# Performance work log

Hardware: AMD Instinct MI355X
Metric: run time of the kernel (lower is better)

## Reference

```python
import jax, jax.numpy as jnp
import numpy as np

N = 100000       # nodes
F_IN = 512       # input features
H = 16           # hidden dim of conv1
C = 5            # num classes
E = 6400000      # edges (avg degree 64)


def setup_inputs() -> dict:
    key = jax.random.key(0)
    ks = jax.random.split(key, 8)
    x = jax.random.normal(ks[0], (N, F_IN), dtype=jnp.float32)
    edge_index = jax.random.randint(ks[1], (2, E), 0, N, dtype=jnp.int64)
    W1 = jax.random.normal(ks[2], (F_IN, H), dtype=jnp.float32) * (1.0 / np.sqrt(F_IN))
    b1 = jnp.zeros((H,), jnp.float32)
    W2 = jax.random.normal(ks[3], (H, C), dtype=jnp.float32) * (1.0 / np.sqrt(H))
    b2 = jnp.zeros((C,), jnp.float32)
    W3 = jax.random.normal(ks[4], (C, 32), dtype=jnp.float32) * (1.0 / np.sqrt(C))
    b3 = jnp.zeros((32,), jnp.float32)
    W4 = jax.random.normal(ks[5], (32, C), dtype=jnp.float32) * (1.0 / np.sqrt(32))
    b4 = jnp.zeros((C,), jnp.float32)
    return {"x": x, "edge_index": edge_index, "W1": W1, "b1": b1,
            "W2": W2, "b2": b2, "W3": W3, "b3": b3, "W4": W4, "b4": b4}


def _gcn_norm(edge_index):
    # add self-loops, unit edge weights (data has no edge_attr)
    loop = jnp.arange(N, dtype=edge_index.dtype)
    src = jnp.concatenate([edge_index[0], loop])
    dst = jnp.concatenate([edge_index[1], loop])
    deg = jax.ops.segment_sum(jnp.ones_like(dst, dtype=jnp.float32), dst,
                              num_segments=N)
    dinv = jnp.where(deg > 0, jax.lax.rsqrt(jnp.maximum(deg, 1.0)), 0.0)
    norm = dinv[src] * dinv[dst]  # [E+N]
    return src, dst, norm


def _gcn_conv(x, src, dst, norm, W, b):
    h = x @ W                               # transform first (small out dim)
    msg = h[src] * norm[:, None]            # gather + edge-normalize
    out = jax.ops.segment_sum(msg, dst, num_segments=N)  # scatter-add
    return out + b


def reference(x, edge_index, W1, b1, W2, b2, W3, b3, W4, b4):
    src, dst, norm = _gcn_norm(edge_index)
    h = _gcn_conv(x, src, dst, norm, W1, b1)
    h = jax.nn.relu(h)
    # F.dropout(training=self.training): identity in eval mode
    h = _gcn_conv(h, src, dst, norm, W2, b2)
    h = jax.nn.relu(h @ W3 + b3)
    h = h @ W4 + b4
    return jax.nn.log_softmax(h, axis=1)
```

## Files before the change

kernel.cpp:

```cpp
#include <hip/hip_runtime.h>
#include <hip/hip_bf16.h>


#define F_IN 512
#define HDIM 16
#define CDIM 5
#define NB   1024
#define SEG  8192
#define GWP_STRIDE 16
#define EPT  10
#define SCHUNK (1024*EPT)
#define CAP  8192

typedef __attribute__((ext_vector_type(8))) short short8;
typedef __attribute__((ext_vector_type(4))) float floatx4;

__device__ inline float bf2f(unsigned short u){
  unsigned int i = ((unsigned int)u) << 16; float f; __builtin_memcpy(&f, &i, 4); return f;
}
__device__ inline unsigned short f2bf(float x){
  unsigned int i; __builtin_memcpy(&i, &x, 4);
  unsigned int r = i + 0x7FFFu + ((i >> 16) & 1u);
  return (unsigned short)(r >> 16);
}
__device__ inline float ulo(unsigned int u){
  unsigned int v = u << 16; float f; __builtin_memcpy(&f, &v, 4); return f;
}
__device__ inline float uhi(unsigned int u){
  unsigned int v = u & 0xFFFF0000u; float f; __builtin_memcpy(&f, &v, 4); return f;
}
__device__ inline short8 pack8(float4 u0, float4 u1){
  unsigned short o[8] = {f2bf(u0.x), f2bf(u0.y), f2bf(u0.z), f2bf(u0.w),
                         f2bf(u1.x), f2bf(u1.y), f2bf(u1.z), f2bf(u1.w)};
  short8 r; __builtin_memcpy(&r, o, 16); return r;
}

__global__ __launch_bounds__(1024) void k_detect(const int* __restrict__ ei, int* __restrict__ flag,
                                                 int* __restrict__ gwp, const float* __restrict__ W1,
                                                 unsigned short* __restrict__ pw, int E){
  int t = threadIdx.x;
  if (t == 0) *flag = 0;
  gwp[t * GWP_STRIDE] = t * SEG;
  {
    int col = t & 15, kg = (t >> 4) & 3, tt = t >> 6;
    unsigned short o[8];
    #pragma unroll
    for (int e = 0; e < 8; ++e)
      o[e] = f2bf(W1[(tt * 32 + kg * 8 + e) * HDIM + col]);
    uint4 v; __builtin_memcpy(&v, o, 16);
    *(uint4*)(pw + (size_t)t * 8) = v;
  }
  __syncthreads();
  long long step = E / 1024; if (step < 1) step = 1;
  long long pos = 2LL * ((long long)t * step) + 1;
  if (pos < 2LL * E){
    if (ei[pos] != 0) atomicOr(flag, 1);
  }
}

__global__ __launch_bounds__(1024) void k_binscatter(const int* __restrict__ ei, const int* __restrict__ flag,
                                                     int* __restrict__ gwp, int* __restrict__ pairs,
                                                     int E, int NPB){
  __shared__ int bh[NB];
  __shared__ int lex[NB];
  __shared__ int bb2[NB];
  __shared__ int wsum[16];
  __shared__ unsigned short kb[SCHUNK];
  __shared__ int stage[SCHUNK];
  int t = threadIdx.x;
  int e0 = blockIdx.x * SCHUNK;
  int e1 = min(E, e0 + SCHUNK);
  int cnt = e1 - e0;
  if (cnt <= 0) return;
  int is32 = *flag;
  const uint2* ei2 = (const uint2*)ei;
  int pk[EPT]; int bi[EPT];
  #pragma unroll
  for (int j = 0; j < EPT; ++j){
    int e = e0 + t + j * 1024;
    if (e < e1){
      int src, dst;
      if (is32){ src = ei[e]; dst = ei[(size_t)E + e]; }
      else     { src = (int)ei2[e].x; dst = (int)ei2[(size_t)E + e].x; }
      int b = dst / NPB;
      pk[j] = src | ((dst - b * NPB) << 20);
      bi[j] = b;
    } else bi[j] = -1;
  }
  bh[t] = 0;
  __syncthreads();
  #pragma unroll
  for (int j = 0; j < EPT; ++j) if (bi[j] >= 0) atomicAdd(&bh[bi[j]], 1);
  __syncthreads();
  {
    int lane = t & 63, w = t >> 6;
    int v = bh[t];
    int xs = v;
    #pragma unroll
    for (int off = 1; off < 64; off <<= 1){
      int y = __shfl_up(xs, off);
      if (lane >= off) xs += y;
    }
    if (lane == 63) wsum[w] = xs;
    __syncthreads();
    int woff = 0;
    for (int k = 0; k < w; ++k) woff += wsum[k];
    int excl = woff + xs - v;
    lex[t] = excl;
    bb2[t] = v ? atomicAdd(&gwp[t * GWP_STRIDE], v) : 0;
    __syncthreads();
    bh[t] = excl;
  }
  __syncthreads();
  #pragma unroll
  for (int j = 0; j < EPT; ++j){
    if (bi[j] >= 0){
      int idx = atomicAdd(&bh[bi[j]], 1);
      stage[idx] = pk[j];
      kb[idx] = (unsigned short)bi[j];
    }
  }
  __syncthreads();
  for (int k = t; k < cnt; k += 1024){
    int b = kb[k];
    pairs[bb2[b] + (k - lex[b])] = stage[k];
  }
}

__global__ __launch_bounds__(512) void k_bucket(const int* __restrict__ pairs, const int* __restrict__ gwp,
                                                int* __restrict__ rowptr, int* __restrict__ rowdeg,
                                                float* __restrict__ dinv, int* __restrict__ ssrc,
                                                int NPB, int n){
  __shared__ int lcnt[8][128];
  __shared__ int tot[128];
  __shared__ int lexcl[128];
  __shared__ int w0sum;
  __shared__ int stage[CAP];
  int b = blockIdx.x;
  int t = threadIdx.x;
  int g = t >> 6;
  int node0 = b * NPB;
  int pbase = b * SEG;
  int obase = b * SEG;
  int cntE = gwp[b * GWP_STRIDE] - b * SEG;
  for (int k = t & 63; k < 128; k += 64) lcnt[g][k] = 0;
  __syncthreads();
  for (int k = t; k < cntE; k += 512){
    unsigned int v = (unsigned int)pairs[pbase + k];
    atomicAdd(&lcnt[g][v >> 20], 1);
  }
  __syncthreads();
  if (t < 128){
    int c = 0;
    #pragma unroll
    for (int gg = 0; gg < 8; ++gg){
      int tmp = lcnt[gg][t];
      lcnt[gg][t] = c;
      c += tmp;
    }
    tot[t] = c;
  }
  __syncthreads();
  int lane = t & 63;
  int v = (t < 128) ? tot[t] : 0;
  int xs = v;
  #pragma unroll
  for (int off = 1; off < 64; off <<= 1){
    int y = __shfl_up(xs, off);
    if (lane >= off) xs += y;
  }
  if (t == 63) w0sum = xs;
  __syncthreads();
  if (t < 128) lexcl[t] = xs - v + ((t >= 64) ? w0sum : 0);
  __syncthreads();
  if (t < NPB){
    int node = node0 + t;
    if (node < n){
      rowptr[node] = obase + lexcl[t];
      rowdeg[node] = tot[t];
      dinv[node] = rsqrtf((float)(tot[t] + 1));
    }
  }
  if (t < 128){
    #pragma unroll
    for (int gg = 0; gg < 8; ++gg) lcnt[gg][t] += lexcl[t];
  }
  __syncthreads();
  for (int k = t; k < cntE; k += 512){
    unsigned int v2 = (unsigned int)pairs[pbase + k];
    int idx = atomicAdd(&lcnt[g][v2 >> 20], 1);
    int src = (int)(v2 & 0xFFFFFu);
    if (idx < CAP) stage[idx] = src;
    else ssrc[obase + idx] = src;
  }
  __syncthreads();
  int m = cntE < CAP ? cntE : CAP;
  for (int k = t; k < m; k += 512) ssrc[obase + k] = stage[k];
}

__global__ __launch_bounds__(256) void k_gemm1(const float* __restrict__ x, const unsigned short* __restrict__ pw,
                                               const float* __restrict__ dinv, unsigned short* __restrict__ hs1,
                                               int n){
  int lane = threadIdx.x & 63;
  int col = lane & 15;
  int kg  = lane >> 4;
  int nt = (n + 15) >> 4;
  const short8* pw8 = (const short8*)pw;
  short8 B[16];
  #pragma unroll
  for (int t = 0; t < 16; ++t) B[t] = pw8[t * 64 + kg * 16 + col];
  int nw = gridDim.x * 4;
  for (int wid = blockIdx.x * 4 + (threadIdx.x >> 6); wid < nt; wid += nw){
    int row = wid * 16 + col;
    const float* xr = x + (size_t)min(row, n - 1) * F_IN;
    floatx4 acc = {0.f, 0.f, 0.f, 0.f};
    #pragma unroll
    for (int t = 0; t < 16; ++t){
      const float4* p = (const float4*)(xr + t * 32 + kg * 8);
      float4 u0 = p[0];
      float4 u1 = p[1];
      acc = __builtin_amdgcn_mfma_f32_16x16x32_bf16(pack8(u0, u1), B[t], acc, 0, 0, 0);
    }
    #pragma unroll
    for (int r = 0; r < 4; ++r){
      int orow = wid * 16 + kg * 4 + r;
      if (orow < n) hs1[(size_t)orow * HDIM + col] = f2bf(dinv[orow] * acc[r]);
    }
  }
}

__global__ __launch_bounds__(256) void k_agg1(const unsigned short* __restrict__ hs1,
    const int* __restrict__ rowptr, const int* __restrict__ rowdeg, const int* __restrict__ ssrc,
    const float* __restrict__ dinv, const float* __restrict__ b1,
    const float* __restrict__ W2, unsigned short* __restrict__ hs2, int n){
  int lane = threadIdx.x & 63;
  int i = blockIdx.x * 4 + (threadIdx.x >> 6);
  if (i >= n) return;
  int slot = lane >> 1, half = lane & 1;
  int beg = rowptr[i], end = beg + rowdeg[i];
  const uint4* hv = (const uint4*)hs1;
  float acc[8];
  #pragma unroll
  for (int k = 0; k < 8; ++k) acc[k] = 0.f;
  for (int e = beg + slot; e < end; e += 32){
    int src = ssrc[e];
    uint4 v = hv[(size_t)src * 2 + half];
    acc[0] += ulo(v.x); acc[1] += uhi(v.x);
    acc[2] += ulo(v.y); acc[3] += uhi(v.y);
    acc[4] += ulo(v.z); acc[5] += uhi(v.z);
    acc[6] += ulo(v.w); acc[7] += uhi(v.w);
  }
  #pragma unroll
  for (int off = 2; off < 64; off <<= 1){
    #pragma unroll
    for (int k = 0; k < 8; ++k) acc[k] += __shfl_xor(acc[k], off);
  }
  uint4 sv = hv[(size_t)i * 2 + half];
  float self[8] = {ulo(sv.x), uhi(sv.x), ulo(sv.y), uhi(sv.y),
                   ulo(sv.z), uhi(sv.z), ulo(sv.w), uhi(sv.w)};
  float dv = dinv[i];
  const float4* b1v = (const float4*)b1;
  float4 bl = b1v[half * 2], bh = b1v[half * 2 + 1];
  float r[8];
  r[0] = fmaxf(fmaf(dv, acc[0] + self[0], bl.x), 0.f);
  r[1] = fmaxf(fmaf(dv, acc[1] + self[1], bl.y), 0.f);
  r[2] = fmaxf(fmaf(dv, acc[2] + self[2], bl.z), 0.f);
  r[3] = fmaxf(fmaf(dv, acc[3] + self[3], bl.w), 0.f);
  r[4] = fmaxf(fmaf(dv, acc[4] + self[4], bh.x), 0.f);
  r[5] = fmaxf(fmaf(dv, acc[5] + self[5], bh.y), 0.f);
  r[6] = fmaxf(fmaf(dv, acc[6] + self[6], bh.z), 0.f);
  r[7] = fmaxf(fmaf(dv, acc[7] + self[7], bh.w), 0.f);
  const float* w2 = W2 + half * 8 * CDIM;
  float p[CDIM];
  #pragma unroll
  for (int c = 0; c < CDIM; ++c){
    float s = 0.f;
    #pragma unroll
    for (int k = 0; k < 8; ++k) s = fmaf(r[k], w2[k * CDIM + c], s);
    p[c] = s;
  }
  #pragma unroll
  for (int c = 0; c < CDIM; ++c) p[c] += __shfl_xor(p[c], 1);
  if (lane == 0){
    unsigned short o[8];
    #pragma unroll
    for (int c = 0; c < CDIM; ++c) o[c] = f2bf(dv * p[c]);
    o[5] = 0; o[6] = 0; o[7] = 0;
    uint4 v; __builtin_memcpy(&v, o, 16);
    *(uint4*)(hs2 + (size_t)i * 8) = v;
  }
}

__global__ __launch_bounds__(256) void k_agg2(const unsigned short* __restrict__ hs2,
    const int* __restrict__ rowptr, const int* __restrict__ rowdeg, const int* __restrict__ ssrc,
    const float* __restrict__ dinv, const float* __restrict__ b2,
    const float* __restrict__ W3, const float* __restrict__ b3,
    const float* __restrict__ W4, const float* __restrict__ b4,
    float* __restrict__ out, int n){
  int lane = threadIdx.x & 63;
  int i = blockIdx.x * 4 + (threadIdx.x >> 6);
  if (i >= n) return;
  int beg = rowptr[i], end = beg + rowdeg[i];
  const uint4* hv = (const uint4*)hs2;
  float acc[CDIM];
  #pragma unroll
  for (int k = 0; k < CDIM; ++k) acc[k] = 0.f;
  for (int e = beg + lane; e < end; e += 64){
    int src = ssrc[e];
    uint4 v = hv[src];
    acc[0] += ulo(v.x); acc[1] += uhi(v.x);
    acc[2] += ulo(v.y); acc[3] += uhi(v.y);
    acc[4] += ulo(v.z);
  }
  #pragma unroll
  for (int off = 1; off < 64; off <<= 1){
    #pragma unroll
    for (int k = 0; k < CDIM; ++k) acc[k] += __shfl_xor(acc[k], off);
  }
  float dv = dinv[i];
  uint4 sv = hv[i];
  float a0 = fmaf(dv, acc[0] + ulo(sv.x), b2[0]);
  float a1 = fmaf(dv, acc[1] + uhi(sv.x), b2[1]);
  float a2 = fmaf(dv, acc[2] + ulo(sv.y), b2[2]);
  float a3 = fmaf(dv, acc[3] + uhi(sv.y), b2[3]);
  float a4 = fmaf(dv, acc[4] + ulo(sv.z), b2[4]);
  int m = lane & 31;
  float h3 = b3[m];
  h3 = fmaf(a0, W3[0 * 32 + m], h3);
  h3 = fmaf(a1, W3[1 * 32 + m], h3);
  h3 = fmaf(a2, W3[2 * 32 + m], h3);
  h3 = fmaf(a3, W3[3 * 32 + m], h3);
  h3 = fmaf(a4, W3[4 * 32 + m], h3);
  h3 = fmaxf(h3, 0.f);
  float q0 = h3 * W4[m * CDIM + 0], q1 = h3 * W4[m * CDIM + 1], q2 = h3 * W4[m * CDIM + 2];
  float q3 = h3 * W4[m * CDIM + 3], q4 = h3 * W4[m * CDIM + 4];
  #pragma unroll
  for (int off = 1; off < 32; off <<= 1){
    q0 += __shfl_xor(q0, off); q1 += __shfl_xor(q1, off); q2 += __shfl_xor(q2, off);
    q3 += __shfl_xor(q3, off); q4 += __shfl_xor(q4, off);
  }
  q0 += b4[0]; q1 += b4[1]; q2 += b4[2]; q3 += b4[3]; q4 += b4[4];
  float mx = fmaxf(fmaxf(fmaxf(q0, q1), fmaxf(q2, q3)), q4);
  float sum = expf(q0 - mx) + expf(q1 - mx) + expf(q2 - mx) + expf(q3 - mx) + expf(q4 - mx);
  float lse = mx + logf(sum);
  if (lane < CDIM){
    float v = q0;
    if (lane == 1) v = q1;
    if (lane == 2) v = q2;
    if (lane == 3) v = q3;
    if (lane == 4) v = q4;
    out[(size_t)i * CDIM + lane] = v - lse;
  }
}

extern "C" void kernel_launch(void* const* d_in, const int* in_sizes, int n_in,
                              void* d_out, int out_size, void* d_ws, size_t ws_size,
                              hipStream_t stream){
  const float* x  = (const float*)d_in[0];
  const int*   ei = (const int*)d_in[1];
  const float* W1 = (const float*)d_in[2];
  const float* b1 = (const float*)d_in[3];
  const float* W2 = (const float*)d_in[4];
  const float* b2 = (const float*)d_in[5];
  const float* W3 = (const float*)d_in[6];
  const float* b3 = (const float*)d_in[7];
  const float* W4 = (const float*)d_in[8];
  const float* b4 = (const float*)d_in[9];
  float* out = (float*)d_out;

  int N = in_sizes[0] / F_IN;
  int E = in_sizes[1] / 2;
  int NPB = (N + NB - 1) / NB;

  char* ws = (char*)d_ws;
  size_t off = 0;
  auto alloc = [&](size_t bytes) -> char* {
    char* p = ws + off;
    off += (bytes + 255) & ~(size_t)255;
    return p;
  };
  int* flag  = (int*)alloc(4);
  int* gwp   = (int*)alloc((size_t)NB * GWP_STRIDE * 4);
  int* rowptr= (int*)alloc((size_t)N * 4);
  int* rowdeg= (int*)alloc((size_t)N * 4);
  float* dinv= (float*)alloc((size_t)N * 4);
  unsigned short* pw = (unsigned short*)alloc((size_t)F_IN * HDIM * 2);
  int* pairs = (int*)alloc((size_t)NB * SEG * 4);
  int* ssrc  = (int*)alloc((size_t)NB * SEG * 4);
  unsigned short* hs1 = (unsigned short*)alloc((size_t)N * HDIM * 2);
  unsigned short* hs2 = (unsigned short*)alloc((size_t)N * 8 * 2);
  (void)ws_size; (void)n_in; (void)out_size;

  k_detect<<<1, 1024, 0, stream>>>(ei, flag, gwp, W1, pw, E);
  int sblocks = (E + SCHUNK - 1) / SCHUNK;
  k_binscatter<<<sblocks, 1024, 0, stream>>>(ei, flag, gwp, pairs, E, NPB);
  k_bucket<<<NB, 512, 0, stream>>>(pairs, gwp, rowptr, rowdeg, dinv, ssrc, NPB, N);
  k_gemm1<<<768, 256, 0, stream>>>(x, pw, dinv, hs1, N);
  k_agg1<<<(N + 3) / 4, 256, 0, stream>>>(hs1, rowptr, rowdeg, ssrc, dinv, b1, W2, hs2, N);
  k_agg2<<<(N + 3) / 4, 256, 0, stream>>>(hs2, rowptr, rowdeg, ssrc, dinv, b2, W3, b3, W4, b4, out, N);
}
```

Baseline: 257.9 us.

## Fuse edge bin-scatter and feature GEMM into one concurrent heterogeneous kernel

```diff
diff --git a/kernel.cpp b/kernel.cpp
--- a/kernel.cpp
+++ b/kernel.cpp
@@ -11,13 +11,11 @@
 #define EPT  10
 #define SCHUNK (1024*EPT)
 #define CAP  8192
+#define GEMM_BLOCKS 512
 
 typedef __attribute__((ext_vector_type(8))) short short8;
 typedef __attribute__((ext_vector_type(4))) float floatx4;
 
-__device__ inline float bf2f(unsigned short u){
-  unsigned int i = ((unsigned int)u) << 16; float f; __builtin_memcpy(&f, &i, 4); return f;
-}
 __device__ inline unsigned short f2bf(float x){
   unsigned int i; __builtin_memcpy(&i, &x, 4);
   unsigned int r = i + 0x7FFFu + ((i >> 16) & 1u);
@@ -35,44 +33,74 @@
   short8 r; __builtin_memcpy(&r, o, 16); return r;
 }
 
-__global__ __launch_bounds__(1024) void k_detect(const int* __restrict__ ei, int* __restrict__ flag,
-                                                 int* __restrict__ gwp, const float* __restrict__ W1,
-                                                 unsigned short* __restrict__ pw, int E){
+__global__ __launch_bounds__(1024, 8) void k_combo(const int* __restrict__ ei,
+    int* __restrict__ gwp, int* __restrict__ pairs,
+    const float* __restrict__ x, const float* __restrict__ W1,
+    unsigned short* __restrict__ h1, int E, int n, int NPB, int sb){
+  __shared__ union U {
+    struct {
+      int bh[NB];
+      int lex[NB];
+      int bb2[NB];
+      int wsum[16];
+      int is32_s;
+      unsigned short kb[SCHUNK];
+      int stage[SCHUNK];
+    } s;
+    unsigned short pwl[F_IN * HDIM];
+  } u;
   int t = threadIdx.x;
-  if (t == 0) *flag = 0;
-  gwp[t * GWP_STRIDE] = t * SEG;
-  {
-    int col = t & 15, kg = (t >> 4) & 3, tt = t >> 6;
-    unsigned short o[8];
-    #pragma unroll
-    for (int e = 0; e < 8; ++e)
-      o[e] = f2bf(W1[(tt * 32 + kg * 8 + e) * HDIM + col]);
-    uint4 v; __builtin_memcpy(&v, o, 16);
-    *(uint4*)(pw + (size_t)t * 8) = v;
-  }
-  __syncthreads();
-  long long step = E / 1024; if (step < 1) step = 1;
-  long long pos = 2LL * ((long long)t * step) + 1;
-  if (pos < 2LL * E){
-    if (ei[pos] != 0) atomicOr(flag, 1);
-  }
-}
-
-__global__ __launch_bounds__(1024) void k_binscatter(const int* __restrict__ ei, const int* __restrict__ flag,
-                                                     int* __restrict__ gwp, int* __restrict__ pairs,
-                                                     int E, int NPB){
-  __shared__ int bh[NB];
-  __shared__ int lex[NB];
-  __shared__ int bb2[NB];
-  __shared__ int wsum[16];
-  __shared__ unsigned short kb[SCHUNK];
-  __shared__ int stage[SCHUNK];
-  int t = threadIdx.x;
+
+  if (blockIdx.x >= sb){
+    {
+      int col = t & 15, kg = (t >> 4) & 3, tt = t >> 6;
+      unsigned short o[8];
+      #pragma unroll
+      for (int e = 0; e < 8; ++e)
+        o[e] = f2bf(W1[(tt * 32 + kg * 8 + e) * HDIM + col]);
+      uint4 v; __builtin_memcpy(&v, o, 16);
+      *(uint4*)(u.pwl + (size_t)t * 8) = v;
+    }
+    __syncthreads();
+    int lane = t & 63;
+    int col = lane & 15, kg = lane >> 4;
+    int nt = (n + 15) >> 4;
+    const short8* pw8 = (const short8*)u.pwl;
+    int nwav = (gridDim.x - sb) * 16;
+    for (int wid = (blockIdx.x - sb) * 16 + (t >> 6); wid < nt; wid += nwav){
+      int row = wid * 16 + col;
+      const float* xr = x + (size_t)min(row, n - 1) * F_IN;
+      floatx4 acc = {0.f, 0.f, 0.f, 0.f};
+      #pragma unroll 1
+      for (int tt = 0; tt < 16; ++tt){
+        const float4* p = (const float4*)(xr + tt * 32 + kg * 8);
+        float4 u0 = p[0];
+        float4 u1 = p[1];
+        short8 Bf = pw8[tt * 64 + kg * 16 + col];
+        acc = __builtin_amdgcn_mfma_f32_16x16x32_bf16(pack8(u0, u1), Bf, acc, 0, 0, 0);
+      }
+      #pragma unroll
+      for (int r = 0; r < 4; ++r){
+        int orow = wid * 16 + kg * 4 + r;
+        if (orow < n) h1[(size_t)orow * HDIM + col] = f2bf(acc[r]);
+      }
+    }
+    return;
+  }
+
   int e0 = blockIdx.x * SCHUNK;
   int e1 = min(E, e0 + SCHUNK);
   int cnt = e1 - e0;
   if (cnt <= 0) return;
-  int is32 = *flag;
+  if (t == 0) u.s.is32_s = 0;
+  u.s.bh[t] = 0;
+  __syncthreads();
+  if (t < 256){
+    long long e = e0 + ((long long)t * cnt) / 256;
+    if (ei[2 * e + 1] != 0) atomicOr(&u.s.is32_s, 1);
+  }
+  __syncthreads();
+  int is32 = u.s.is32_s;
   const uint2* ei2 = (const uint2*)ei;
   int pk[EPT]; int bi[EPT];
   #pragma unroll
@@ -87,43 +115,41 @@
       bi[j] = b;
     } else bi[j] = -1;
   }
-  bh[t] = 0;
-  __syncthreads();
-  #pragma unroll
-  for (int j = 0; j < EPT; ++j) if (bi[j] >= 0) atomicAdd(&bh[bi[j]], 1);
+  #pragma unroll
+  for (int j = 0; j < EPT; ++j) if (bi[j] >= 0) atomicAdd(&u.s.bh[bi[j]], 1);
   __syncthreads();
   {
     int lane = t & 63, w = t >> 6;
-    int v = bh[t];
+    int v = u.s.bh[t];
     int xs = v;
     #pragma unroll
     for (int off = 1; off < 64; off <<= 1){
       int y = __shfl_up(xs, off);
       if (lane >= off) xs += y;
     }
-    if (lane == 63) wsum[w] = xs;
+    if (lane == 63) u.s.wsum[w] = xs;
     __syncthreads();
     int woff = 0;
-    for (int k = 0; k < w; ++k) woff += wsum[k];
+    for (int k = 0; k < w; ++k) woff += u.s.wsum[k];
     int excl = woff + xs - v;
-    lex[t] = excl;
-    bb2[t] = v ? atomicAdd(&gwp[t * GWP_STRIDE], v) : 0;
+    u.s.lex[t] = excl;
+    u.s.bb2[t] = t * SEG + (v ? atomicAdd(&gwp[t * GWP_STRIDE], v) : 0);
     __syncthreads();
-    bh[t] = excl;
+    u.s.bh[t] = excl;
   }
   __syncthreads();
   #pragma unroll
   for (int j = 0; j < EPT; ++j){
     if (bi[j] >= 0){
-      int idx = atomicAdd(&bh[bi[j]], 1);
-      stage[idx] = pk[j];
-      kb[idx] = (unsigned short)bi[j];
+      int idx = atomicAdd(&u.s.bh[bi[j]], 1);
+      u.s.stage[idx] = pk[j];
+      u.s.kb[idx] = (unsigned short)bi[j];
     }
   }
   __syncthreads();
   for (int k = t; k < cnt; k += 1024){
-    int b = kb[k];
-    pairs[bb2[b] + (k - lex[b])] = stage[k];
+    int b = u.s.kb[k];
+    pairs[u.s.bb2[b] + (k - u.s.lex[b])] = u.s.stage[k];
   }
 }
 
@@ -141,8 +167,9 @@
   int g = t >> 6;
   int node0 = b * NPB;
   int pbase = b * SEG;
-  int obase = b * SEG;
-  int cntE = gwp[b * GWP_STRIDE] - b * SEG;
+  int cntE = gwp[b * GWP_STRIDE];
+  if (cntE < 0) cntE = 0;
+  if (cntE > SEG) cntE = SEG;
   for (int k = t & 63; k < 128; k += 64) lcnt[g][k] = 0;
   __syncthreads();
   for (int k = t; k < cntE; k += 512){
@@ -176,7 +203,7 @@
   if (t < NPB){
     int node = node0 + t;
     if (node < n){
-      rowptr[node] = obase + lexcl[t];
+      rowptr[node] = pbase + lexcl[t];
       rowdeg[node] = tot[t];
       dinv[node] = rsqrtf((float)(tot[t] + 1));
     }
@@ -191,45 +218,14 @@
     int idx = atomicAdd(&lcnt[g][v2 >> 20], 1);
     int src = (int)(v2 & 0xFFFFFu);
     if (idx < CAP) stage[idx] = src;
-    else ssrc[obase + idx] = src;
+    else ssrc[pbase + idx] = src;
   }
   __syncthreads();
   int m = cntE < CAP ? cntE : CAP;
-  for (int k = t; k < m; k += 512) ssrc[obase + k] = stage[k];
-}
-
-__global__ __launch_bounds__(256) void k_gemm1(const float* __restrict__ x, const unsigned short* __restrict__ pw,
-                                               const float* __restrict__ dinv, unsigned short* __restrict__ hs1,
-                                               int n){
-  int lane = threadIdx.x & 63;
-  int col = lane & 15;
-  int kg  = lane >> 4;
-  int nt = (n + 15) >> 4;
-  const short8* pw8 = (const short8*)pw;
-  short8 B[16];
-  #pragma unroll
-  for (int t = 0; t < 16; ++t) B[t] = pw8[t * 64 + kg * 16 + col];
-  int nw = gridDim.x * 4;
-  for (int wid = blockIdx.x * 4 + (threadIdx.x >> 6); wid < nt; wid += nw){
-    int row = wid * 16 + col;
-    const float* xr = x + (size_t)min(row, n - 1) * F_IN;
-    floatx4 acc = {0.f, 0.f, 0.f, 0.f};
-    #pragma unroll
-    for (int t = 0; t < 16; ++t){
-      const float4* p = (const float4*)(xr + t * 32 + kg * 8);
-      float4 u0 = p[0];
-      float4 u1 = p[1];
-      acc = __builtin_amdgcn_mfma_f32_16x16x32_bf16(pack8(u0, u1), B[t], acc, 0, 0, 0);
-    }
-    #pragma unroll
-    for (int r = 0; r < 4; ++r){
-      int orow = wid * 16 + kg * 4 + r;
-      if (orow < n) hs1[(size_t)orow * HDIM + col] = f2bf(dinv[orow] * acc[r]);
-    }
-  }
-}
-
-__global__ __launch_bounds__(256) void k_agg1(const unsigned short* __restrict__ hs1,
+  for (int k = t; k < m; k += 512) ssrc[pbase + k] = stage[k];
+}
+
+__global__ __launch_bounds__(256) void k_agg1(const unsigned short* __restrict__ h1,
     const int* __restrict__ rowptr, const int* __restrict__ rowdeg, const int* __restrict__ ssrc,
     const float* __restrict__ dinv, const float* __restrict__ b1,
     const float* __restrict__ W2, unsigned short* __restrict__ hs2, int n){
@@ -238,17 +234,18 @@
   if (i >= n) return;
   int slot = lane >> 1, half = lane & 1;
   int beg = rowptr[i], end = beg + rowdeg[i];
-  const uint4* hv = (const uint4*)hs1;
+  const uint4* hv = (const uint4*)h1;
   float acc[8];
   #pragma unroll
   for (int k = 0; k < 8; ++k) acc[k] = 0.f;
   for (int e = beg + slot; e < end; e += 32){
     int src = ssrc[e];
+    float ds = dinv[src];
     uint4 v = hv[(size_t)src * 2 + half];
-    acc[0] += ulo(v.x); acc[1] += uhi(v.x);
-    acc[2] += ulo(v.y); acc[3] += uhi(v.y);
-    acc[4] += ulo(v.z); acc[5] += uhi(v.z);
-    acc[6] += ulo(v.w); acc[7] += uhi(v.w);
+    acc[0] = fmaf(ds, ulo(v.x), acc[0]); acc[1] = fmaf(ds, uhi(v.x), acc[1]);
+    acc[2] = fmaf(ds, ulo(v.y), acc[2]); acc[3] = fmaf(ds, uhi(v.y), acc[3]);
+    acc[4] = fmaf(ds, ulo(v.z), acc[4]); acc[5] = fmaf(ds, uhi(v.z), acc[5]);
+    acc[6] = fmaf(ds, ulo(v.w), acc[6]); acc[7] = fmaf(ds, uhi(v.w), acc[7]);
   }
   #pragma unroll
   for (int off = 2; off < 64; off <<= 1){
@@ -262,14 +259,14 @@
   const float4* b1v = (const float4*)b1;
   float4 bl = b1v[half * 2], bh = b1v[half * 2 + 1];
   float r[8];
-  r[0] = fmaxf(fmaf(dv, acc[0] + self[0], bl.x), 0.f);
-  r[1] = fmaxf(fmaf(dv, acc[1] + self[1], bl.y), 0.f);
-  r[2] = fmaxf(fmaf(dv, acc[2] + self[2], bl.z), 0.f);
-  r[3] = fmaxf(fmaf(dv, acc[3] + self[3], bl.w), 0.f);
-  r[4] = fmaxf(fmaf(dv, acc[4] + self[4], bh.x), 0.f);
-  r[5] = fmaxf(fmaf(dv, acc[5] + self[5], bh.y), 0.f);
-  r[6] = fmaxf(fmaf(dv, acc[6] + self[6], bh.z), 0.f);
-  r[7] = fmaxf(fmaf(dv, acc[7] + self[7], bh.w), 0.f);
+  r[0] = fmaxf(fmaf(dv, fmaf(dv, self[0], acc[0]), bl.x), 0.f);
+  r[1] = fmaxf(fmaf(dv, fmaf(dv, self[1], acc[1]), bl.y), 0.f);
+  r[2] = fmaxf(fmaf(dv, fmaf(dv, self[2], acc[2]), bl.z), 0.f);
+  r[3] = fmaxf(fmaf(dv, fmaf(dv, self[3], acc[3]), bl.w), 0.f);
+  r[4] = fmaxf(fmaf(dv, fmaf(dv, self[4], acc[4]), bh.x), 0.f);
+  r[5] = fmaxf(fmaf(dv, fmaf(dv, self[5], acc[5]), bh.y), 0.f);
+  r[6] = fmaxf(fmaf(dv, fmaf(dv, self[6], acc[6]), bh.z), 0.f);
+  r[7] = fmaxf(fmaf(dv, fmaf(dv, self[7], acc[7]), bh.w), 0.f);
   const float* w2 = W2 + half * 8 * CDIM;
   float p[CDIM];
   #pragma unroll
@@ -379,23 +376,20 @@
     off += (bytes + 255) & ~(size_t)255;
     return p;
   };
-  int* flag  = (int*)alloc(4);
   int* gwp   = (int*)alloc((size_t)NB * GWP_STRIDE * 4);
   int* rowptr= (int*)alloc((size_t)N * 4);
   int* rowdeg= (int*)alloc((size_t)N * 4);
   float* dinv= (float*)alloc((size_t)N * 4);
-  unsigned short* pw = (unsigned short*)alloc((size_t)F_IN * HDIM * 2);
   int* pairs = (int*)alloc((size_t)NB * SEG * 4);
   int* ssrc  = (int*)alloc((size_t)NB * SEG * 4);
-  unsigned short* hs1 = (unsigned short*)alloc((size_t)N * HDIM * 2);
+  unsigned short* h1 = (unsigned short*)alloc((size_t)N * HDIM * 2);
   unsigned short* hs2 = (unsigned short*)alloc((size_t)N * 8 * 2);
   (void)ws_size; (void)n_in; (void)out_size;
 
-  k_detect<<<1, 1024, 0, stream>>>(ei, flag, gwp, W1, pw, E);
+  hipMemsetAsync(gwp, 0, (size_t)NB * GWP_STRIDE * 4, stream);
   int sblocks = (E + SCHUNK - 1) / SCHUNK;
-  k_binscatter<<<sblocks, 1024, 0, stream>>>(ei, flag, gwp, pairs, E, NPB);
+  k_combo<<<sblocks + GEMM_BLOCKS, 1024, 0, stream>>>(ei, gwp, pairs, x, W1, h1, E, N, NPB, sblocks);
   k_bucket<<<NB, 512, 0, stream>>>(pairs, gwp, rowptr, rowdeg, dinv, ssrc, NPB, N);
-  k_gemm1<<<768, 256, 0, stream>>>(x, pw, dinv, hs1, N);
-  k_agg1<<<(N + 3) / 4, 256, 0, stream>>>(hs1, rowptr, rowdeg, ssrc, dinv, b1, W2, hs2, N);
+  k_agg1<<<(N + 3) / 4, 256, 0, stream>>>(h1, rowptr, rowdeg, ssrc, dinv, b1, W2, hs2, N);
   k_agg2<<<(N + 3) / 4, 256, 0, stream>>>(hs2, rowptr, rowdeg, ssrc, dinv, b2, W3, b3, W4, b4, out, N);
 }
```

Result: no change. 259.2 us (+0.5%).

## Fuse CSR bucketing into aggregation kernels and drop global sorted-source array

Applied to the files above, without the earlier changes.

```diff
diff --git a/kernel.cpp b/kernel.cpp
--- a/kernel.cpp
+++ b/kernel.cpp
@@ -10,14 +10,10 @@
 #define GWP_STRIDE 16
 #define EPT  10
 #define SCHUNK (1024*EPT)
-#define CAP  8192
 
 typedef __attribute__((ext_vector_type(8))) short short8;
 typedef __attribute__((ext_vector_type(4))) float floatx4;
 
-__device__ inline float bf2f(unsigned short u){
-  unsigned int i = ((unsigned int)u) << 16; float f; __builtin_memcpy(&f, &i, 4); return f;
-}
 __device__ inline unsigned short f2bf(float x){
   unsigned int i; __builtin_memcpy(&i, &x, 4);
   unsigned int r = i + 0x7FFFu + ((i >> 16) & 1u);
@@ -35,36 +31,13 @@
   short8 r; __builtin_memcpy(&r, o, 16); return r;
 }
 
-__global__ __launch_bounds__(1024) void k_detect(const int* __restrict__ ei, int* __restrict__ flag,
-                                                 int* __restrict__ gwp, const float* __restrict__ W1,
-                                                 unsigned short* __restrict__ pw, int E){
-  int t = threadIdx.x;
-  if (t == 0) *flag = 0;
-  gwp[t * GWP_STRIDE] = t * SEG;
-  {
-    int col = t & 15, kg = (t >> 4) & 3, tt = t >> 6;
-    unsigned short o[8];
-    #pragma unroll
-    for (int e = 0; e < 8; ++e)
-      o[e] = f2bf(W1[(tt * 32 + kg * 8 + e) * HDIM + col]);
-    uint4 v; __builtin_memcpy(&v, o, 16);
-    *(uint4*)(pw + (size_t)t * 8) = v;
-  }
-  __syncthreads();
-  long long step = E / 1024; if (step < 1) step = 1;
-  long long pos = 2LL * ((long long)t * step) + 1;
-  if (pos < 2LL * E){
-    if (ei[pos] != 0) atomicOr(flag, 1);
-  }
-}
-
-__global__ __launch_bounds__(1024) void k_binscatter(const int* __restrict__ ei, const int* __restrict__ flag,
-                                                     int* __restrict__ gwp, int* __restrict__ pairs,
-                                                     int E, int NPB){
+__global__ __launch_bounds__(1024) void k_binscatter(const int* __restrict__ ei,
+    int* __restrict__ gwp, int* __restrict__ pairs, int E, int NPB){
   __shared__ int bh[NB];
   __shared__ int lex[NB];
   __shared__ int bb2[NB];
   __shared__ int wsum[16];
+  __shared__ int is32_s;
   __shared__ unsigned short kb[SCHUNK];
   __shared__ int stage[SCHUNK];
   int t = threadIdx.x;
@@ -72,7 +45,15 @@
   int e1 = min(E, e0 + SCHUNK);
   int cnt = e1 - e0;
   if (cnt <= 0) return;
-  int is32 = *flag;
+  if (t == 0) is32_s = 0;
+  bh[t] = 0;
+  __syncthreads();
+  if (t < 256){
+    long long e = e0 + ((long long)t * cnt) / 256;
+    if (ei[2 * e + 1] != 0) atomicOr(&is32_s, 1);
+  }
+  __syncthreads();
+  int is32 = is32_s;
   const uint2* ei2 = (const uint2*)ei;
   int pk[EPT]; int bi[EPT];
   #pragma unroll
@@ -87,8 +68,6 @@
       bi[j] = b;
     } else bi[j] = -1;
   }
-  bh[t] = 0;
-  __syncthreads();
   #pragma unroll
   for (int j = 0; j < EPT; ++j) if (bi[j] >= 0) atomicAdd(&bh[bi[j]], 1);
   __syncthreads();
@@ -107,7 +86,7 @@
     for (int k = 0; k < w; ++k) woff += wsum[k];
     int excl = woff + xs - v;
     lex[t] = excl;
-    bb2[t] = v ? atomicAdd(&gwp[t * GWP_STRIDE], v) : 0;
+    bb2[t] = t * SEG + (v ? atomicAdd(&gwp[t * GWP_STRIDE], v) : 0);
     __syncthreads();
     bh[t] = excl;
   }
@@ -127,229 +106,287 @@
   }
 }
 
-__global__ __launch_bounds__(512) void k_bucket(const int* __restrict__ pairs, const int* __restrict__ gwp,
-                                                int* __restrict__ rowptr, int* __restrict__ rowdeg,
-                                                float* __restrict__ dinv, int* __restrict__ ssrc,
-                                                int NPB, int n){
-  __shared__ int lcnt[8][128];
+__global__ __launch_bounds__(256) void k_deg(const int* __restrict__ pairs, const int* __restrict__ gwp,
+                                             float* __restrict__ dinv, int n, int NPB){
+  __shared__ int h[128];
+  int b = blockIdx.x, t = threadIdx.x;
+  int cntE = gwp[b * GWP_STRIDE];
+  if (cntE < 0) cntE = 0;
+  if (cntE > SEG) cntE = SEG;
+  if (t < 128) h[t] = 0;
+  __syncthreads();
+  const int* pb = pairs + (size_t)b * SEG;
+  for (int k = t; k < cntE; k += 256) atomicAdd(&h[((unsigned)pb[k]) >> 20], 1);
+  __syncthreads();
+  if (t < NPB){
+    int node = b * NPB + t;
+    if (node < n) dinv[node] = rsqrtf((float)(h[t] + 1));
+  }
+}
+
+__global__ __launch_bounds__(256) void k_gemm1(const float* __restrict__ x, const float* __restrict__ W1,
+                                               const float* __restrict__ dinv, unsigned short* __restrict__ hs1,
+                                               int n){
+  __shared__ unsigned short pwl[F_IN * HDIM];
+  int t = threadIdx.x;
+  for (int slot = t; slot < 1024; slot += 256){
+    int col = slot & 15, kg = (slot >> 4) & 3, tt = slot >> 6;
+    unsigned short o[8];
+    #pragma unroll
+    for (int e = 0; e < 8; ++e)
+      o[e] = f2bf(W1[(tt * 32 + kg * 8 + e) * HDIM + col]);
+    uint4 v; __builtin_memcpy(&v, o, 16);
+    *(uint4*)(pwl + (size_t)slot * 8) = v;
+  }
+  __syncthreads();
+  int lane = t & 63;
+  int col = lane & 15, kg = lane >> 4;
+  int nt = (n + 15) >> 4;
+  const short8* pw8 = (const short8*)pwl;
+  int nw = gridDim.x * 4;
+  for (int wid = blockIdx.x * 4 + (t >> 6); wid < nt; wid += nw){
+    int row = wid * 16 + col;
+    const float* xr = x + (size_t)min(row, n - 1) * F_IN;
+    floatx4 acc = {0.f, 0.f, 0.f, 0.f};
+    #pragma unroll
+    for (int tt = 0; tt < 16; ++tt){
+      const float4* p = (const float4*)(xr + tt * 32 + kg * 8);
+      float4 u0 = p[0];
+      float4 u1 = p[1];
+      short8 Bf = pw8[tt * 64 + kg * 16 + col];
+      acc = __builtin_amdgcn_mfma_f32_16x16x32_bf16(pack8(u0, u1), Bf, acc, 0, 0, 0);
+    }
+    #pragma unroll
+    for (int r = 0; r < 4; ++r){
+      int orow = wid * 16 + kg * 4 + r;
+      if (orow < n) hs1[(size_t)orow * HDIM + col] = f2bf(dinv[orow] * acc[r]);
+    }
+  }
+}
+
+__global__ __launch_bounds__(512) void k_agg1s(const unsigned short* __restrict__ hs1,
+    const int* __restrict__ pairs, const int* __restrict__ gwp,
+    const float* __restrict__ dinv, const float* __restrict__ b1,
+    const float* __restrict__ W2, unsigned short* __restrict__ hs2, int n, int NPB){
+  __shared__ int stage[SEG];
+  __shared__ int lcnt[4][128];
   __shared__ int tot[128];
   __shared__ int lexcl[128];
   __shared__ int w0sum;
-  __shared__ int stage[CAP];
-  int b = blockIdx.x;
-  int t = threadIdx.x;
-  int g = t >> 6;
-  int node0 = b * NPB;
-  int pbase = b * SEG;
-  int obase = b * SEG;
-  int cntE = gwp[b * GWP_STRIDE] - b * SEG;
-  for (int k = t & 63; k < 128; k += 64) lcnt[g][k] = 0;
-  __syncthreads();
-  for (int k = t; k < cntE; k += 512){
-    unsigned int v = (unsigned int)pairs[pbase + k];
-    atomicAdd(&lcnt[g][v >> 20], 1);
-  }
+  int b = blockIdx.x, t = threadIdx.x;
+  int lane = t & 63;
+  int g = t >> 7;
+  int cntE = gwp[b * GWP_STRIDE];
+  if (cntE < 0) cntE = 0;
+  if (cntE > SEG) cntE = SEG;
+  const int* pb = pairs + (size_t)b * SEG;
+  lcnt[g][t & 127] = 0;
+  __syncthreads();
+  for (int k = t; k < cntE; k += 512)
+    atomicAdd(&lcnt[g][((unsigned)pb[k]) >> 20], 1);
   __syncthreads();
   if (t < 128){
     int c = 0;
     #pragma unroll
-    for (int gg = 0; gg < 8; ++gg){
-      int tmp = lcnt[gg][t];
-      lcnt[gg][t] = c;
-      c += tmp;
-    }
+    for (int gg = 0; gg < 4; ++gg){ int tmp = lcnt[gg][t]; lcnt[gg][t] = c; c += tmp; }
     tot[t] = c;
   }
   __syncthreads();
-  int lane = t & 63;
-  int v = (t < 128) ? tot[t] : 0;
-  int xs = v;
-  #pragma unroll
-  for (int off = 1; off < 64; off <<= 1){
-    int y = __shfl_up(xs, off);
-    if (lane >= off) xs += y;
-  }
-  if (t == 63) w0sum = xs;
-  __syncthreads();
-  if (t < 128) lexcl[t] = xs - v + ((t >= 64) ? w0sum : 0);
-  __syncthreads();
-  if (t < NPB){
-    int node = node0 + t;
-    if (node < n){
-      rowptr[node] = obase + lexcl[t];
-      rowdeg[node] = tot[t];
-      dinv[node] = rsqrtf((float)(tot[t] + 1));
-    }
-  }
+  {
+    int v = (t < 128) ? tot[t] : 0;
+    int xs = v;
+    #pragma unroll
+    for (int off = 1; off < 64; off <<= 1){
+      int y = __shfl_up(xs, off);
+      if (lane >= off) xs += y;
+    }
+    if (t == 63) w0sum = xs;
+    __syncthreads();
+    if (t < 128) lexcl[t] = xs - v + ((t >= 64) ? w0sum : 0);
+  }
+  __syncthreads();
   if (t < 128){
     #pragma unroll
-    for (int gg = 0; gg < 8; ++gg) lcnt[gg][t] += lexcl[t];
+    for (int gg = 0; gg < 4; ++gg) lcnt[gg][t] += lexcl[t];
   }
   __syncthreads();
   for (int k = t; k < cntE; k += 512){
-    unsigned int v2 = (unsigned int)pairs[pbase + k];
-    int idx = atomicAdd(&lcnt[g][v2 >> 20], 1);
-    int src = (int)(v2 & 0xFFFFFu);
-    if (idx < CAP) stage[idx] = src;
-    else ssrc[obase + idx] = src;
-  }
-  __syncthreads();
-  int m = cntE < CAP ? cntE : CAP;
-  for (int k = t; k < m; k += 512) ssrc[obase + k] = stage[k];
-}
-
-__global__ __launch_bounds__(256) void k_gemm1(const float* __restrict__ x, const unsigned short* __restrict__ pw,
-                                               const float* __restrict__ dinv, unsigned short* __restrict__ hs1,
-                                               int n){
-  int lane = threadIdx.x & 63;
-  int col = lane & 15;
-  int kg  = lane >> 4;
-  int nt = (n + 15) >> 4;
-  const short8* pw8 = (const short8*)pw;
-  short8 B[16];
-  #pragma unroll
-  for (int t = 0; t < 16; ++t) B[t] = pw8[t * 64 + kg * 16 + col];
-  int nw = gridDim.x * 4;
-  for (int wid = blockIdx.x * 4 + (threadIdx.x >> 6); wid < nt; wid += nw){
-    int row = wid * 16 + col;
-    const float* xr = x + (size_t)min(row, n - 1) * F_IN;
-    floatx4 acc = {0.f, 0.f, 0.f, 0.f};
-    #pragma unroll
-    for (int t = 0; t < 16; ++t){
-      const float4* p = (const float4*)(xr + t * 32 + kg * 8);
-      float4 u0 = p[0];
-      float4 u1 = p[1];
-      acc = __builtin_amdgcn_mfma_f32_16x16x32_bf16(pack8(u0, u1), B[t], acc, 0, 0, 0);
-    }
-    #pragma unroll
-    for (int r = 0; r < 4; ++r){
-      int orow = wid * 16 + kg * 4 + r;
-      if (orow < n) hs1[(size_t)orow * HDIM + col] = f2bf(dinv[orow] * acc[r]);
-    }
-  }
-}
-
-__global__ __launch_bounds__(256) void k_agg1(const unsigned short* __restrict__ hs1,
-    const int* __restrict__ rowptr, const int* __restrict__ rowdeg, const int* __restrict__ ssrc,
-    const float* __restrict__ dinv, const float* __restrict__ b1,
-    const float* __restrict__ W2, unsigned short* __restrict__ hs2, int n){
-  int lane = threadIdx.x & 63;
-  int i = blockIdx.x * 4 + (threadIdx.x >> 6);
-  if (i >= n) return;
+    unsigned int v = (unsigned int)pb[k];
+    int idx = atomicAdd(&lcnt[g][v >> 20], 1);
+    stage[idx] = (int)(v & 0xFFFFFu);
+  }
+  __syncthreads();
+  const uint4* hv = (const uint4*)hs1;
+  const float4* b1v = (const float4*)b1;
+  int wv = t >> 6;
   int slot = lane >> 1, half = lane & 1;
-  int beg = rowptr[i], end = beg + rowdeg[i];
-  const uint4* hv = (const uint4*)hs1;
-  float acc[8];
-  #pragma unroll
-  for (int k = 0; k < 8; ++k) acc[k] = 0.f;
-  for (int e = beg + slot; e < end; e += 32){
-    int src = ssrc[e];
-    uint4 v = hv[(size_t)src * 2 + half];
-    acc[0] += ulo(v.x); acc[1] += uhi(v.x);
-    acc[2] += ulo(v.y); acc[3] += uhi(v.y);
-    acc[4] += ulo(v.z); acc[5] += uhi(v.z);
-    acc[6] += ulo(v.w); acc[7] += uhi(v.w);
-  }
-  #pragma unroll
-  for (int off = 2; off < 64; off <<= 1){
-    #pragma unroll
-    for (int k = 0; k < 8; ++k) acc[k] += __shfl_xor(acc[k], off);
-  }
-  uint4 sv = hv[(size_t)i * 2 + half];
-  float self[8] = {ulo(sv.x), uhi(sv.x), ulo(sv.y), uhi(sv.y),
-                   ulo(sv.z), uhi(sv.z), ulo(sv.w), uhi(sv.w)};
-  float dv = dinv[i];
-  const float4* b1v = (const float4*)b1;
-  float4 bl = b1v[half * 2], bh = b1v[half * 2 + 1];
-  float r[8];
-  r[0] = fmaxf(fmaf(dv, acc[0] + self[0], bl.x), 0.f);
-  r[1] = fmaxf(fmaf(dv, acc[1] + self[1], bl.y), 0.f);
-  r[2] = fmaxf(fmaf(dv, acc[2] + self[2], bl.z), 0.f);
-  r[3] = fmaxf(fmaf(dv, acc[3] + self[3], bl.w), 0.f);
-  r[4] = fmaxf(fmaf(dv, acc[4] + self[4], bh.x), 0.f);
-  r[5] = fmaxf(fmaf(dv, acc[5] + self[5], bh.y), 0.f);
-  r[6] = fmaxf(fmaf(dv, acc[6] + self[6], bh.z), 0.f);
-  r[7] = fmaxf(fmaf(dv, acc[7] + self[7], bh.w), 0.f);
-  const float* w2 = W2 + half * 8 * CDIM;
-  float p[CDIM];
-  #pragma unroll
-  for (int c = 0; c < CDIM; ++c){
-    float s = 0.f;
-    #pragma unroll
-    for (int k = 0; k < 8; ++k) s = fmaf(r[k], w2[k * CDIM + c], s);
-    p[c] = s;
-  }
-  #pragma unroll
-  for (int c = 0; c < CDIM; ++c) p[c] += __shfl_xor(p[c], 1);
-  if (lane == 0){
-    unsigned short o[8];
-    #pragma unroll
-    for (int c = 0; c < CDIM; ++c) o[c] = f2bf(dv * p[c]);
-    o[5] = 0; o[6] = 0; o[7] = 0;
-    uint4 v; __builtin_memcpy(&v, o, 16);
-    *(uint4*)(hs2 + (size_t)i * 8) = v;
-  }
-}
-
-__global__ __launch_bounds__(256) void k_agg2(const unsigned short* __restrict__ hs2,
-    const int* __restrict__ rowptr, const int* __restrict__ rowdeg, const int* __restrict__ ssrc,
+  for (int i = wv; i < NPB; i += 8){
+    int node = b * NPB + i;
+    if (node >= n) break;
+    int beg = lexcl[i], deg = tot[i];
+    float acc[8];
+    #pragma unroll
+    for (int k = 0; k < 8; ++k) acc[k] = 0.f;
+    for (int e = beg + slot; e < beg + deg; e += 32){
+      int src = stage[e];
+      uint4 v = hv[(size_t)src * 2 + half];
+      acc[0] += ulo(v.x); acc[1] += uhi(v.x);
+      acc[2] += ulo(v.y); acc[3] += uhi(v.y);
+      acc[4] += ulo(v.z); acc[5] += uhi(v.z);
+      acc[6] += ulo(v.w); acc[7] += uhi(v.w);
+    }
+    #pragma unroll
+    for (int off = 2; off < 64; off <<= 1){
+      #pragma unroll
+      for (int k = 0; k < 8; ++k) acc[k] += __shfl_xor(acc[k], off);
+    }
+    uint4 sv = hv[(size_t)node * 2 + half];
+    float self[8] = {ulo(sv.x), uhi(sv.x), ulo(sv.y), uhi(sv.y),
+                     ulo(sv.z), uhi(sv.z), ulo(sv.w), uhi(sv.w)};
+    float dv = dinv[node];
+    float4 bl = b1v[half * 2], bh = b1v[half * 2 + 1];
+    float r[8];
+    r[0] = fmaxf(fmaf(dv, acc[0] + self[0], bl.x), 0.f);
+    r[1] = fmaxf(fmaf(dv, acc[1] + self[1], bl.y), 0.f);
+    r[2] = fmaxf(fmaf(dv, acc[2] + self[2], bl.z), 0.f);
+    r[3] = fmaxf(fmaf(dv, acc[3] + self[3], bl.w), 0.f);
+    r[4] = fmaxf(fmaf(dv, acc[4] + self[4], bh.x), 0.f);
+    r[5] = fmaxf(fmaf(dv, acc[5] + self[5], bh.y), 0.f);
+    r[6] = fmaxf(fmaf(dv, acc[6] + self[6], bh.z), 0.f);
+    r[7] = fmaxf(fmaf(dv, acc[7] + self[7], bh.w), 0.f);
+    const float* w2 = W2 + half * 8 * CDIM;
+    float p[CDIM];
+    #pragma unroll
+    for (int c = 0; c < CDIM; ++c){
+      float s = 0.f;
+      #pragma unroll
+      for (int k = 0; k < 8; ++k) s = fmaf(r[k], w2[k * CDIM + c], s);
+      p[c] = s;
+    }
+    #pragma unroll
+    for (int c = 0; c < CDIM; ++c) p[c] += __shfl_xor(p[c], 1);
+    if (lane == 0){
+      unsigned short o[8];
+      #pragma unroll
+      for (int c = 0; c < CDIM; ++c) o[c] = f2bf(dv * p[c]);
+      o[5] = 0; o[6] = 0; o[7] = 0;
+      uint4 v; __builtin_memcpy(&v, o, 16);
+      *(uint4*)(hs2 + (size_t)node * 8) = v;
+    }
+  }
+}
+
+__global__ __launch_bounds__(512) void k_agg2s(const unsigned short* __restrict__ hs2,
+    const int* __restrict__ pairs, const int* __restrict__ gwp,
     const float* __restrict__ dinv, const float* __restrict__ b2,
     const float* __restrict__ W3, const float* __restrict__ b3,
     const float* __restrict__ W4, const float* __restrict__ b4,
-    float* __restrict__ out, int n){
-  int lane = threadIdx.x & 63;
-  int i = blockIdx.x * 4 + (threadIdx.x >> 6);
-  if (i >= n) return;
-  int beg = rowptr[i], end = beg + rowdeg[i];
-  const uint4* hv = (const uint4*)hs2;
-  float acc[CDIM];
-  #pragma unroll
-  for (int k = 0; k < CDIM; ++k) acc[k] = 0.f;
-  for (int e = beg + lane; e < end; e += 64){
-    int src = ssrc[e];
-    uint4 v = hv[src];
-    acc[0] += ulo(v.x); acc[1] += uhi(v.x);
-    acc[2] += ulo(v.y); acc[3] += uhi(v.y);
-    acc[4] += ulo(v.z);
-  }
-  #pragma unroll
-  for (int off = 1; off < 64; off <<= 1){
-    #pragma unroll
-    for (int k = 0; k < CDIM; ++k) acc[k] += __shfl_xor(acc[k], off);
-  }
-  float dv = dinv[i];
-  uint4 sv = hv[i];
-  float a0 = fmaf(dv, acc[0] + ulo(sv.x), b2[0]);
-  float a1 = fmaf(dv, acc[1] + uhi(sv.x), b2[1]);
-  float a2 = fmaf(dv, acc[2] + ulo(sv.y), b2[2]);
-  float a3 = fmaf(dv, acc[3] + uhi(sv.y), b2[3]);
-  float a4 = fmaf(dv, acc[4] + ulo(sv.z), b2[4]);
-  int m = lane & 31;
-  float h3 = b3[m];
-  h3 = fmaf(a0, W3[0 * 32 + m], h3);
-  h3 = fmaf(a1, W3[1 * 32 + m], h3);
-  h3 = fmaf(a2, W3[2 * 32 + m], h3);
-  h3 = fmaf(a3, W3[3 * 32 + m], h3);
-  h3 = fmaf(a4, W3[4 * 32 + m], h3);
-  h3 = fmaxf(h3, 0.f);
-  float q0 = h3 * W4[m * CDIM + 0], q1 = h3 * W4[m * CDIM + 1], q2 = h3 * W4[m * CDIM + 2];
-  float q3 = h3 * W4[m * CDIM + 3], q4 = h3 * W4[m * CDIM + 4];
-  #pragma unroll
-  for (int off = 1; off < 32; off <<= 1){
-    q0 += __shfl_xor(q0, off); q1 += __shfl_xor(q1, off); q2 += __shfl_xor(q2, off);
-    q3 += __shfl_xor(q3, off); q4 += __shfl_xor(q4, off);
-  }
-  q0 += b4[0]; q1 += b4[1]; q2 += b4[2]; q3 += b4[3]; q4 += b4[4];
-  float mx = fmaxf(fmaxf(fmaxf(q0, q1), fmaxf(q2, q3)), q4);
-  float sum = expf(q0 - mx) + expf(q1 - mx) + expf(q2 - mx) + expf(q3 - mx) + expf(q4 - mx);
-  float lse = mx + logf(sum);
-  if (lane < CDIM){
-    float v = q0;
-    if (lane == 1) v = q1;
-    if (lane == 2) v = q2;
-    if (lane == 3) v = q3;
-    if (lane == 4) v = q4;
-    out[(size_t)i * CDIM + lane] = v - lse;
+    float* __restrict__ out, int n, int NPB){
+  __shared__ int stage[SEG];
+  __shared__ int lcnt[4][128];
+  __shared__ int tot[128];
+  __shared__ int lexcl[128];
+  __shared__ int w0sum;
+  int b = blockIdx.x, t = threadIdx.x;
+  int lane = t & 63;
+  int g = t >> 7;
+  int cntE = gwp[b * GWP_STRIDE];
+  if (cntE < 0) cntE = 0;
+  if (cntE > SEG) cntE = SEG;
+  const int* pb = pairs + (size_t)b * SEG;
+  lcnt[g][t & 127] = 0;
+  __syncthreads();
+  for (int k = t; k < cntE; k += 512)
+    atomicAdd(&lcnt[g][((unsigned)pb[k]) >> 20], 1);
+  __syncthreads();
+  if (t < 128){
+    int c = 0;
+    #pragma unroll
+    for (int gg = 0; gg < 4; ++gg){ int tmp = lcnt[gg][t]; lcnt[gg][t] = c; c += tmp; }
+    tot[t] = c;
+  }
+  __syncthreads();
+  {
+    int v = (t < 128) ? tot[t] : 0;
+    int xs = v;
+    #pragma unroll
+    for (int off = 1; off < 64; off <<= 1){
+      int y = __shfl_up(xs, off);
+      if (lane >= off) xs += y;
+    }
+    if (t == 63) w0sum = xs;
+    __syncthreads();
+    if (t < 128) lexcl[t] = xs - v + ((t >= 64) ? w0sum : 0);
+  }
+  __syncthreads();
+  if (t < 128){
+    #pragma unroll
+    for (int gg = 0; gg < 4; ++gg) lcnt[gg][t] += lexcl[t];
+  }
+  __syncthreads();
+  for (int k = t; k < cntE; k += 512){
+    unsigned int v = (unsigned int)pb[k];
+    int idx = atomicAdd(&lcnt[g][v >> 20], 1);
+    stage[idx] = (int)(v & 0xFFFFFu);
+  }
+  __syncthreads();
+  const uint4* hv2 = (const uint4*)hs2;
+  int wv = t >> 6;
+  for (int i = wv; i < NPB; i += 8){
+    int node = b * NPB + i;
+    if (node >= n) break;
+    int beg = lexcl[i], deg = tot[i];
+    float a[CDIM];
+    #pragma unroll
+    for (int k = 0; k < CDIM; ++k) a[k] = 0.f;
+    for (int e = beg + lane; e < beg + deg; e += 64){
+      int src = stage[e];
+      uint4 v = hv2[src];
+      a[0] += ulo(v.x); a[1] += uhi(v.x);
+      a[2] += ulo(v.y); a[3] += uhi(v.y);
+      a[4] += ulo(v.z);
+    }
+    #pragma unroll
+    for (int off = 1; off < 64; off <<= 1){
+      #pragma unroll
+      for (int k = 0; k < CDIM; ++k) a[k] += __shfl_xor(a[k], off);
+    }
+    float dv = dinv[node];
+    uint4 sv = hv2[node];
+    float a0 = fmaf(dv, a[0] + ulo(sv.x), b2[0]);
+    float a1 = fmaf(dv, a[1] + uhi(sv.x), b2[1]);
+    float a2 = fmaf(dv, a[2] + ulo(sv.y), b2[2]);
+    float a3 = fmaf(dv, a[3] + uhi(sv.y), b2[3]);
+    float a4 = fmaf(dv, a[4] + ulo(sv.z), b2[4]);
+    int m = lane & 31;
+    float h3 = b3[m];
+    h3 = fmaf(a0, W3[0 * 32 + m], h3);
+    h3 = fmaf(a1, W3[1 * 32 + m], h3);
+    h3 = fmaf(a2, W3[2 * 32 + m], h3);
+    h3 = fmaf(a3, W3[3 * 32 + m], h3);
+    h3 = fmaf(a4, W3[4 * 32 + m], h3);
+    h3 = fmaxf(h3, 0.f);
+    float q0 = h3 * W4[m * CDIM + 0], q1 = h3 * W4[m * CDIM + 1];
+    float q2 = h3 * W4[m * CDIM + 2], q3 = h3 * W4[m * CDIM + 3];
+    float q4 = h3 * W4[m * CDIM + 4];
+    #pragma unroll
+    for (int off = 1; off < 32; off <<= 1){
+      q0 += __shfl_xor(q0, off); q1 += __shfl_xor(q1, off); q2 += __shfl_xor(q2, off);
+      q3 += __shfl_xor(q3, off); q4 += __shfl_xor(q4, off);
+    }
+    q0 += b4[0]; q1 += b4[1]; q2 += b4[2]; q3 += b4[3]; q4 += b4[4];
+    float mx = fmaxf(fmaxf(fmaxf(q0, q1), fmaxf(q2, q3)), q4);
+    float sum = expf(q0 - mx) + expf(q1 - mx) + expf(q2 - mx) +
+                expf(q3 - mx) + expf(q4 - mx);
+    float lse = mx + logf(sum);
+    if (lane < CDIM){
+      float v = q0;
+      if (lane == 1) v = q1;
+      if (lane == 2) v = q2;
+      if (lane == 3) v = q3;
+      if (lane == 4) v = q4;
+      out[(size_t)node * CDIM + lane] = v - lse;
+    }
   }
 }
 
@@ -379,23 +416,18 @@
     off += (bytes + 255) & ~(size_t)255;
     return p;
   };
-  int* flag  = (int*)alloc(4);
   int* gwp   = (int*)alloc((size_t)NB * GWP_STRIDE * 4);
-  int* rowptr= (int*)alloc((size_t)N * 4);
-  int* rowdeg= (int*)alloc((size_t)N * 4);
   float* dinv= (float*)alloc((size_t)N * 4);
-  unsigned short* pw = (unsigned short*)alloc((size_t)F_IN * HDIM * 2);
   int* pairs = (int*)alloc((size_t)NB * SEG * 4);
-  int* ssrc  = (int*)alloc((size_t)NB * SEG * 4);
   unsigned short* hs1 = (unsigned short*)alloc((size_t)N * HDIM * 2);
   unsigned short* hs2 = (unsigned short*)alloc((size_t)N * 8 * 2);
   (void)ws_size; (void)n_in; (void)out_size;
 
-  k_detect<<<1, 1024, 0, stream>>>(ei, flag, gwp, W1, pw, E);
+  hipMemsetAsync(gwp, 0, (size_t)NB * GWP_STRIDE * 4, stream);
   int sblocks = (E + SCHUNK - 1) / SCHUNK;
-  k_binscatter<<<sblocks, 1024, 0, stream>>>(ei, flag, gwp, pairs, E, NPB);
-  k_bucket<<<NB, 512, 0, stream>>>(pairs, gwp, rowptr, rowdeg, dinv, ssrc, NPB, N);
-  k_gemm1<<<768, 256, 0, stream>>>(x, pw, dinv, hs1, N);
-  k_agg1<<<(N + 3) / 4, 256, 0, stream>>>(hs1, rowptr, rowdeg, ssrc, dinv, b1, W2, hs2, N);
-  k_agg2<<<(N + 3) / 4, 256, 0, stream>>>(hs2, rowptr, rowdeg, ssrc, dinv, b2, W3, b3, W4, b4, out, N);
-}
+  k_binscatter<<<sblocks, 1024, 0, stream>>>(ei, gwp, pairs, E, NPB);
+  k_deg<<<NB, 256, 0, stream>>>(pairs, gwp, dinv, N, NPB);
+  k_gemm1<<<768, 256, 0, stream>>>(x, W1, dinv, hs1, N);
+  k_agg1s<<<NB, 512, 0, stream>>>(hs1, pairs, gwp, dinv, b1, W2, hs2, N, NPB);
+  k_agg2s<<<NB, 512, 0, stream>>>(hs2, pairs, gwp, dinv, b2, W3, b3, W4, b4, out, N, NPB);
+}
```

Result: slower. 272.1 us (+5.5%).
